# Kernel tuning notes

Hardware: AMD Instinct MI355X
Metric: run time of the kernel (lower is better)

Reference implementation:

```python
import jax, jax.numpy as jnp
import numpy as np

B, X, H = 2048, 1024, 1024
DR = 0.5

def setup_inputs() -> dict:
    key = jax.random.key(0)
    ks = jax.random.split(key, 21)
    std = 1.0 / np.sqrt(H)
    u = lambda k, s: jax.random.uniform(k, s, jnp.float32, -std, std)
    bern = lambda k, s: (jax.random.bernoulli(k, 1.0 - DR, s) / (1.0 - DR)).astype(jnp.float32)
    return {
        "x": jax.random.normal(ks[0], (B, X), jnp.float32),
        "h0": jax.random.normal(ks[1], (B, H), jnp.float32),
        "c0": jax.random.normal(ks[2], (B, H), jnp.float32),
        "w_xi": u(ks[3], (H, X)), "w_xf": u(ks[4], (H, X)),
        "w_xc": u(ks[5], (H, X)), "w_xo": u(ks[6], (H, X)),
        "w_hi": u(ks[7], (H, H)), "w_hf": u(ks[8], (H, H)),
        "w_hc": u(ks[9], (H, H)), "w_ho": u(ks[10], (H, H)),
        "b_i": u(ks[11], (H,)), "b_f": u(ks[12], (H,)),
        "b_c": u(ks[13], (H,)), "b_o": u(ks[14], (H,)),
        "maskHI": bern(ks[15], (B, H)), "maskHF": bern(ks[16], (B, H)),
        "maskHC": bern(ks[17], (B, H)), "maskHO": bern(ks[18], (B, H)),
        "maskC": bern(ks[19], (B, H)),
    }

def reference(x, h0, c0,
              w_xi, w_xf, w_xc, w_xo,
              w_hi, w_hf, w_hc, w_ho,
              b_i, b_f, b_c, b_o,
              maskHI, maskHF, maskHC, maskHO, maskC):
    # gal dropout: per-gate masks on recurrent input h0
    hs = jnp.stack([h0 * maskHI, h0 * maskHF, h0 * maskHC, h0 * maskHO])  # [4,B,H]
    wh = jnp.stack([w_hi, w_hf, w_hc, w_ho])                              # [4,H,H]
    wx = jnp.stack([w_xi, w_xf, w_xc, w_xo])                              # [4,H,X]
    # two batched GEMMs (F.linear uses x @ W.T)
    g = jnp.einsum('bx,gkx->gbk', x, wx) + jnp.einsum('gbh,gkh->gbk', hs, wh)
    gateI = jax.nn.sigmoid(g[0] + b_i)
    gateF = jax.nn.sigmoid(g[1] + b_f)
    gateC = jnp.tanh(g[2] + b_c) * maskC   # sem dropout on candidate
    gateO = jax.nn.sigmoid(g[3] + b_o)
    c1 = gateF * c0 + gateI * gateC
    h1 = gateO * jnp.tanh(c1)
    return (h1, c1)
```

## Files before the change

kernel.cpp:

```cpp
#include <hip/hip_runtime.h>
#include <hip/hip_bf16.h>
#include <stdint.h>

#define BDIM 2048
#define HDIM 1024
#define XDIM 1024
#define BH (BDIM*HDIM)
#define WSEG 1048576

typedef __attribute__((ext_vector_type(8))) short short8;
typedef __attribute__((ext_vector_type(4))) float float4v;

__device__ __forceinline__ void gload16(const void* g, void* l) {
    __builtin_amdgcn_global_load_lds(
        (const __attribute__((address_space(1))) unsigned int*)g,
        (__attribute__((address_space(3))) unsigned int*)l, 16, 0, 0);
}

__device__ __forceinline__ unsigned pack2(float a, float b) {
    __hip_bfloat162 v = __float22bfloat162_rn(make_float2(a, b));
    return *reinterpret_cast<unsigned*>(&v);
}
__device__ __forceinline__ uint2 pack4(float4 f) {
    return make_uint2(pack2(f.x, f.y), pack2(f.z, f.w));
}
__device__ __forceinline__ float2 up2(unsigned u) {
    __hip_bfloat162 v = *reinterpret_cast<__hip_bfloat162*>(&u);
    return __bfloat1622float2(v);
}

__global__ __launch_bounds__(256) void prep_all_k(
    const float* __restrict__ w0, const float* __restrict__ w1,
    const float* __restrict__ w2, const float* __restrict__ w3,
    const float* __restrict__ w4, const float* __restrict__ w5,
    const float* __restrict__ w6, const float* __restrict__ w7,
    const float* __restrict__ x, const float* __restrict__ h0,
    const float* __restrict__ mI, const float* __restrict__ mF,
    const float* __restrict__ mC, const float* __restrict__ mO,
    uint2* __restrict__ dst) {
    const int seg = blockIdx.y;
    const int i = blockIdx.x * 256 + threadIdx.x;
    float4 f;
    if (seg < 10) {
        const float* base;
        switch (seg) {
            case 0: base = w0; break; case 1: base = w1; break;
            case 2: base = w2; break; case 3: base = w3; break;
            case 4: base = w4; break; case 5: base = w5; break;
            case 6: base = w6; break; case 7: base = w7; break;
            default: base = x + (size_t)(seg - 8) * WSEG; break;
        }
        f = ((const float4*)base)[i];
    } else {
        const int s = seg - 10;
        const int g = s >> 1, half = s & 1;
        const float* mp = (g == 0) ? mI : (g == 1) ? mF : (g == 2) ? mC : mO;
        float4 h = ((const float4*)(h0 + (size_t)half * WSEG))[i];
        float4 m = ((const float4*)(mp + (size_t)half * WSEG))[i];
        f = make_float4(h.x * m.x, h.y * m.y, h.z * m.z, h.w * m.w);
    }
    dst[(size_t)seg * (WSEG / 4) + i] = pack4(f);
}

__global__ __launch_bounds__(256, 4) void gemm_split(
    const __hip_bfloat16* __restrict__ ws18,
    __hip_bfloat16* __restrict__ part) {
    const int z = blockIdx.z;
    const int g = z >> 1, half = z & 1;
    const __hip_bfloat16* Ap = half ? (ws18 + (size_t)(10 + 2 * g) * WSEG)
                                    : (ws18 + (size_t)8 * WSEG);
    const __hip_bfloat16* Bp = half ? (ws18 + (size_t)(4 + g) * WSEG)
                                    : (ws18 + (size_t)g * WSEG);

    __shared__ __hip_bfloat16 As[128 * 32];
    __shared__ __hip_bfloat16 Bs[128 * 32];

    const int t = threadIdx.x;
    const int m0 = blockIdx.x * 128;
    const int n0 = blockIdx.y * 128;
    const int wv = t >> 6, lane = t & 63;
    const int wm = (wv >> 1) * 64, wn = (wv & 1) * 64;
    const int quad = lane >> 4, lrow = lane & 15;

    float4v acc[4][4];
#pragma unroll
    for (int i = 0; i < 4; ++i)
#pragma unroll
        for (int j = 0; j < 4; ++j) acc[i][j] = (float4v){0.f, 0.f, 0.f, 0.f};

    const short8* As8 = (const short8*)As;
    const short8* Bs8 = (const short8*)Bs;

    for (int k0 = 0; k0 < 1024; k0 += 32) {
#pragma unroll
        for (int it = 0; it < 2; ++it) {
            int chunk = it * 256 + t;
            int row = chunk >> 2, cc = chunk & 3;
            gload16(Ap + (size_t)(m0 + row) * 1024 + k0 + cc * 8,
                    (char*)As + chunk * 16);
            gload16(Bp + (size_t)(n0 + row) * 1024 + k0 + cc * 8,
                    (char*)Bs + chunk * 16);
        }
        __syncthreads();

        short8 af[4], bfr[4];
#pragma unroll
        for (int mt = 0; mt < 4; ++mt) af[mt] = As8[(wm + mt * 16 + lrow) * 4 + quad];
#pragma unroll
        for (int nt = 0; nt < 4; ++nt) bfr[nt] = Bs8[(wn + nt * 16 + lrow) * 4 + quad];
#pragma unroll
        for (int mt = 0; mt < 4; ++mt)
#pragma unroll
            for (int nt = 0; nt < 4; ++nt)
                acc[mt][nt] = __builtin_amdgcn_mfma_f32_16x16x32_bf16(
                    af[mt], bfr[nt], acc[mt][nt], 0, 0, 0);
        __syncthreads();
    }

    __hip_bfloat16* pz = part + (size_t)z * BH;
#pragma unroll
    for (int nt = 0; nt < 4; ++nt) {
        int col = n0 + wn + nt * 16 + lrow;
#pragma unroll
        for (int mt = 0; mt < 4; ++mt) {
#pragma unroll
            for (int r = 0; r < 4; ++r) {
                int row = m0 + wm + mt * 16 + quad * 4 + r;
                pz[(size_t)row * HDIM + col] = __float2bfloat16(acc[mt][nt][r]);
            }
        }
    }
}

__global__ __launch_bounds__(256) void combine_k(
    const uint2* __restrict__ part,
    const float* __restrict__ bi, const float* __restrict__ bff,
    const float* __restrict__ bc, const float* __restrict__ bo,
    const float* __restrict__ c0, const float* __restrict__ mC,
    float4* __restrict__ out) {
    const int i = blockIdx.x * 256 + threadIdx.x;
    const int h4 = (i * 4 & (HDIM - 1)) >> 2;

    float gate[4][4];
#pragma unroll
    for (int g = 0; g < 4; ++g) {
        uint2 p0 = part[(size_t)(2 * g) * (BH / 4) + i];
        uint2 p1 = part[(size_t)(2 * g + 1) * (BH / 4) + i];
        float2 a0 = up2(p0.x), a1 = up2(p0.y);
        float2 b0 = up2(p1.x), b1 = up2(p1.y);
        gate[g][0] = a0.x + b0.x;
        gate[g][1] = a0.y + b0.y;
        gate[g][2] = a1.x + b1.x;
        gate[g][3] = a1.y + b1.y;
    }
    float4 vbi = ((const float4*)bi)[h4];
    float4 vbf = ((const float4*)bff)[h4];
    float4 vbc = ((const float4*)bc)[h4];
    float4 vbo = ((const float4*)bo)[h4];
    float4 vc0 = ((const float4*)c0)[i];
    float4 vmc = ((const float4*)mC)[i];
    const float* pbi = (const float*)&vbi;
    const float* pbf = (const float*)&vbf;
    const float* pbc = (const float*)&vbc;
    const float* pbo = (const float*)&vbo;
    const float* pc0 = (const float*)&vc0;
    const float* pmc = (const float*)&vmc;

    float h1[4], c1[4];
#pragma unroll
    for (int j = 0; j < 4; ++j) {
        float xi = gate[0][j] + pbi[j];
        float xf = gate[1][j] + pbf[j];
        float xc = gate[2][j] + pbc[j];
        float xo = gate[3][j] + pbo[j];
        float I = 1.f / (1.f + __expf(-xi));
        float F = 1.f / (1.f + __expf(-xf));
        float C = tanhf(xc) * pmc[j];
        float O = 1.f / (1.f + __expf(-xo));
        c1[j] = F * pc0[j] + I * C;
        h1[j] = O * tanhf(c1[j]);
    }
    out[i] = make_float4(h1[0], h1[1], h1[2], h1[3]);
    out[BH / 4 + i] = make_float4(c1[0], c1[1], c1[2], c1[3]);
}

extern "C" void kernel_launch(void* const* d_in, const int* in_sizes, int n_in,
                              void* d_out, int out_size, void* d_ws, size_t ws_size,
                              hipStream_t stream) {
    const float* x   = (const float*)d_in[0];
    const float* h0  = (const float*)d_in[1];
    const float* c0  = (const float*)d_in[2];
    const float* wxi = (const float*)d_in[3];
    const float* wxf = (const float*)d_in[4];
    const float* wxc = (const float*)d_in[5];
    const float* wxo = (const float*)d_in[6];
    const float* whi = (const float*)d_in[7];
    const float* whf = (const float*)d_in[8];
    const float* whc = (const float*)d_in[9];
    const float* who = (const float*)d_in[10];
    const float* bi  = (const float*)d_in[11];
    const float* bf  = (const float*)d_in[12];
    const float* bc  = (const float*)d_in[13];
    const float* bo  = (const float*)d_in[14];
    const float* mI  = (const float*)d_in[15];
    const float* mF  = (const float*)d_in[16];
    const float* mC  = (const float*)d_in[17];
    const float* mO  = (const float*)d_in[18];
    const float* mCell = (const float*)d_in[19];

    __hip_bfloat16* ws18 = (__hip_bfloat16*)d_ws;
    __hip_bfloat16* part = ws18 + (size_t)18 * WSEG;

    prep_all_k<<<dim3(WSEG / 4 / 256, 18), dim3(256), 0, stream>>>(
        wxi, wxf, wxc, wxo, whi, whf, whc, who, x, h0, mI, mF, mC, mO,
        (uint2*)ws18);

    gemm_split<<<dim3(BDIM / 128, HDIM / 128, 8), dim3(256), 0, stream>>>(
        ws18, part);

    combine_k<<<dim3(BH / 4 / 256), dim3(256), 0, stream>>>(
        (const uint2*)part, bi, bf, bc, bo, c0, mCell, (float4*)d_out);
}
```

Before: 213.9 us.

## Fuse activation bf16 conversion and dropout masking into GEMM A-tile load

```diff
diff --git a/kernel.cpp b/kernel.cpp
--- a/kernel.cpp
+++ b/kernel.cpp
@@ -29,48 +29,36 @@
     return __bfloat1622float2(v);
 }
 
-__global__ __launch_bounds__(256) void prep_all_k(
+__global__ __launch_bounds__(256) void prep_w_k(
     const float* __restrict__ w0, const float* __restrict__ w1,
     const float* __restrict__ w2, const float* __restrict__ w3,
     const float* __restrict__ w4, const float* __restrict__ w5,
     const float* __restrict__ w6, const float* __restrict__ w7,
+    uint2* __restrict__ dst) {
+    const int seg = blockIdx.y;
+    const int i = blockIdx.x * 256 + threadIdx.x;
+    const float* base;
+    switch (seg) {
+        case 0: base = w0; break; case 1: base = w1; break;
+        case 2: base = w2; break; case 3: base = w3; break;
+        case 4: base = w4; break; case 5: base = w5; break;
+        case 6: base = w6; break; default: base = w7; break;
+    }
+    float4 f = ((const float4*)base)[i];
+    dst[(size_t)seg * (WSEG / 4) + i] = pack4(f);
+}
+
+__global__ __launch_bounds__(256, 4) void gemm_split(
+    const __hip_bfloat16* __restrict__ wsw,
     const float* __restrict__ x, const float* __restrict__ h0,
     const float* __restrict__ mI, const float* __restrict__ mF,
     const float* __restrict__ mC, const float* __restrict__ mO,
-    uint2* __restrict__ dst) {
-    const int seg = blockIdx.y;
-    const int i = blockIdx.x * 256 + threadIdx.x;
-    float4 f;
-    if (seg < 10) {
-        const float* base;
-        switch (seg) {
-            case 0: base = w0; break; case 1: base = w1; break;
-            case 2: base = w2; break; case 3: base = w3; break;
-            case 4: base = w4; break; case 5: base = w5; break;
-            case 6: base = w6; break; case 7: base = w7; break;
-            default: base = x + (size_t)(seg - 8) * WSEG; break;
-        }
-        f = ((const float4*)base)[i];
-    } else {
-        const int s = seg - 10;
-        const int g = s >> 1, half = s & 1;
-        const float* mp = (g == 0) ? mI : (g == 1) ? mF : (g == 2) ? mC : mO;
-        float4 h = ((const float4*)(h0 + (size_t)half * WSEG))[i];
-        float4 m = ((const float4*)(mp + (size_t)half * WSEG))[i];
-        f = make_float4(h.x * m.x, h.y * m.y, h.z * m.z, h.w * m.w);
-    }
-    dst[(size_t)seg * (WSEG / 4) + i] = pack4(f);
-}
-
-__global__ __launch_bounds__(256, 4) void gemm_split(
-    const __hip_bfloat16* __restrict__ ws18,
     __hip_bfloat16* __restrict__ part) {
     const int z = blockIdx.z;
     const int g = z >> 1, half = z & 1;
-    const __hip_bfloat16* Ap = half ? (ws18 + (size_t)(10 + 2 * g) * WSEG)
-                                    : (ws18 + (size_t)8 * WSEG);
-    const __hip_bfloat16* Bp = half ? (ws18 + (size_t)(4 + g) * WSEG)
-                                    : (ws18 + (size_t)g * WSEG);
+    const float* Afp = half ? h0 : x;
+    const float* Mfp = (g == 0) ? mI : (g == 1) ? mF : (g == 2) ? mC : mO;
+    const __hip_bfloat16* Bp = wsw + (size_t)(half ? (4 + g) : g) * WSEG;
 
     __shared__ __hip_bfloat16 As[128 * 32];
     __shared__ __hip_bfloat16 Bs[128 * 32];
@@ -90,16 +78,31 @@
 
     const short8* As8 = (const short8*)As;
     const short8* Bs8 = (const short8*)Bs;
+    uint4* As16 = (uint4*)As;
 
     for (int k0 = 0; k0 < 1024; k0 += 32) {
 #pragma unroll
         for (int it = 0; it < 2; ++it) {
             int chunk = it * 256 + t;
             int row = chunk >> 2, cc = chunk & 3;
-            gload16(Ap + (size_t)(m0 + row) * 1024 + k0 + cc * 8,
-                    (char*)As + chunk * 16);
             gload16(Bp + (size_t)(n0 + row) * 1024 + k0 + cc * 8,
                     (char*)Bs + chunk * 16);
+        }
+#pragma unroll
+        for (int it = 0; it < 2; ++it) {
+            int chunk = it * 256 + t;
+            int row = chunk >> 2, cc = chunk & 3;
+            size_t off = (size_t)(m0 + row) * 1024 + k0 + cc * 8;
+            float4 a0 = *(const float4*)(Afp + off);
+            float4 a1 = *(const float4*)(Afp + off + 4);
+            if (half) {
+                float4 q0 = *(const float4*)(Mfp + off);
+                float4 q1 = *(const float4*)(Mfp + off + 4);
+                a0 = make_float4(a0.x * q0.x, a0.y * q0.y, a0.z * q0.z, a0.w * q0.w);
+                a1 = make_float4(a1.x * q1.x, a1.y * q1.y, a1.z * q1.z, a1.w * q1.w);
+            }
+            As16[chunk] = make_uint4(pack2(a0.x, a0.y), pack2(a0.z, a0.w),
+                                     pack2(a1.x, a1.y), pack2(a1.z, a1.w));
         }
         __syncthreads();
 
@@ -208,15 +211,14 @@
     const float* mO  = (const float*)d_in[18];
     const float* mCell = (const float*)d_in[19];
 
-    __hip_bfloat16* ws18 = (__hip_bfloat16*)d_ws;
-    __hip_bfloat16* part = ws18 + (size_t)18 * WSEG;
-
-    prep_all_k<<<dim3(WSEG / 4 / 256, 18), dim3(256), 0, stream>>>(
-        wxi, wxf, wxc, wxo, whi, whf, whc, who, x, h0, mI, mF, mC, mO,
-        (uint2*)ws18);
+    __hip_bfloat16* wsw = (__hip_bfloat16*)d_ws;
+    __hip_bfloat16* part = wsw + (size_t)8 * WSEG;
+
+    prep_w_k<<<dim3(WSEG / 4 / 256, 8), dim3(256), 0, stream>>>(
+        wxi, wxf, wxc, wxo, whi, whf, whc, who, (uint2*)wsw);
 
     gemm_split<<<dim3(BDIM / 128, HDIM / 128, 8), dim3(256), 0, stream>>>(
-        ws18, part);
+        wsw, x, h0, mI, mF, mC, mO, part);
 
     combine_k<<<dim3(BH / 4 / 256), dim3(256), 0, stream>>>(
         (const uint2*)part, bi, bf, bc, bo, c0, mCell, (float4*)d_out);
```

Measured after the change: 264.7 us. +23.8%, slower.
